# Performance work log

Measured on AMD Instinct MI355X. Metric: run time of the kernel, lower is better.

Reference implementation:

```python
import jax, jax.numpy as jnp
import numpy as np

B, N, D = 2048, 64, 256
DH = D // 2  # theta/phi projection dim
EPS = 1e-5

def layer_norm(x, g, b):
    m = jnp.mean(x, axis=-1, keepdims=True)
    v = jnp.var(x, axis=-1, keepdims=True)
    return (x - m) * jax.lax.rsqrt(v + EPS) * g + b

def graph_conv(x, adj, th_w, ph_w, fc_w, fc_b):
    # static adjacency: softmax over rows, shared across batch
    A_static = jax.nn.softmax(adj, axis=-1)  # [N, N]
    q = jnp.einsum('bnd,hd->bnh', x, th_w)   # [B, N, DH]
    k = jnp.einsum('bnd,hd->bnh', x, ph_w)   # [B, N, DH]
    scores = jnp.einsum('bni,bmi->bnm', q, k) / jnp.sqrt(jnp.asarray(DH, x.dtype))
    A_hat = A_static[None] + jax.nn.softmax(scores, axis=-1)  # [B, N, N]
    agg = jnp.einsum('bnm,bmd->bnd', A_hat, x)
    return jnp.einsum('bnd,od->bno', agg, fc_w) + fc_b

def setup_inputs() -> dict:
    key = jax.random.key(0)
    ks = jax.random.split(key, 12)
    eye = jnp.eye(N, dtype=jnp.float32)
    s = 1.0 / np.sqrt(D)
    return {
        'graph':  jax.random.normal(ks[0], (B, N, D), jnp.float32),
        'ln_in_g': jnp.ones((D,), jnp.float32), 'ln_in_b': jnp.zeros((D,), jnp.float32),
        'adj0':  eye + 0.01 * jax.random.normal(ks[1], (N, N), jnp.float32),
        'th0':   jax.random.uniform(ks[2], (DH, D), jnp.float32, -s, s),
        'ph0':   jax.random.uniform(ks[3], (DH, D), jnp.float32, -s, s),
        'fcw0':  jax.random.uniform(ks[4], (D, D), jnp.float32, -s, s),
        'fcb0':  jax.random.uniform(ks[5], (D,), jnp.float32, -s, s),
        'ln0_g': jnp.ones((D,), jnp.float32), 'ln0_b': jnp.zeros((D,), jnp.float32),
        'adj1':  eye + 0.01 * jax.random.normal(ks[6], (N, N), jnp.float32),
        'th1':   jax.random.uniform(ks[7], (DH, D), jnp.float32, -s, s),
        'ph1':   jax.random.uniform(ks[8], (DH, D), jnp.float32, -s, s),
        'fcw1':  jax.random.uniform(ks[9], (D, D), jnp.float32, -s, s),
        'fcb1':  jax.random.uniform(ks[10], (D,), jnp.float32, -s, s),
    }

def reference(graph, ln_in_g, ln_in_b, adj0, th0, ph0, fcw0, fcb0,
              ln0_g, ln0_b, adj1, th1, ph1, fcw1, fcb1):
    x = layer_norm(graph, ln_in_g, ln_in_b)
    x = graph_conv(x, adj0, th0, ph0, fcw0, fcb0)
    x = layer_norm(x, ln0_g, ln0_b)
    x = jnp.where(x >= 0, x, 0.1 * x)  # LeakyReLU(0.1); dropout is identity in eval
    x = graph_conv(x, adj1, th1, ph1, fcw1, fcb1)
    return x
```

## Files before the change

kernel.cpp:

```cpp
#include <hip/hip_runtime.h>

typedef __bf16 bf16x8 __attribute__((ext_vector_type(8)));
typedef __bf16 bf16x4 __attribute__((ext_vector_type(4)));
typedef float  f32x4  __attribute__((ext_vector_type(4)));

constexpr int WS_AS0 = 0;
constexpr int WS_AS1 = 4096;
constexpr int WS_TH0 = 8192;
constexpr int WS_PH0 = 40960;
constexpr int WS_FC0 = 73728;
constexpr int WS_TH1 = 139264;
constexpr int WS_PH1 = 172032;
constexpr int WS_FC1 = 204800;

static __device__ __forceinline__ f32x4 mfma16(bf16x8 a, bf16x8 b, f32x4 c) {
    return __builtin_amdgcn_mfma_f32_16x16x32_bf16(a, b, c, 0, 0, 0);
}

__global__ void prep_adj(const float* __restrict__ adj0,
                         const float* __restrict__ adj1,
                         __bf16* __restrict__ wsb) {
    const int t = threadIdx.x;
    const int l = t >> 6, r = t & 63;
    const float* a = (l ? adj1 : adj0) + r * 64;
    float mx = -3.0e38f;
    for (int c = 0; c < 64; ++c) mx = fmaxf(mx, a[c]);
    float s = 0.f;
    for (int c = 0; c < 64; ++c) s += __expf(a[c] - mx);
    const float inv = 1.f / s;
    __bf16* dst = wsb + (l ? WS_AS1 : WS_AS0) + r * 64;
    for (int c = 0; c < 64; ++c) dst[c] = (__bf16)(__expf(a[c] - mx) * inv);
}

__global__ void prep_w(const float* __restrict__ th0, const float* __restrict__ ph0,
                       const float* __restrict__ fc0, const float* __restrict__ th1,
                       const float* __restrict__ ph1, const float* __restrict__ fc1,
                       __bf16* __restrict__ wsb) {
    int i = blockIdx.x * 256 + threadIdx.x;
    if (i >= 262144) return;
    float v; int d;
    if      (i <  32768) { v = th0[i];          d = WS_TH0 + i;          }
    else if (i <  65536) { v = ph0[i -  32768]; d = WS_PH0 + i -  32768; }
    else if (i < 131072) { v = fc0[i -  65536]; d = WS_FC0 + i -  65536; }
    else if (i < 163840) { v = th1[i - 131072]; d = WS_TH1 + i - 131072; }
    else if (i < 196608) { v = ph1[i - 163840]; d = WS_PH1 + i - 163840; }
    else                 { v = fc1[i - 196608]; d = WS_FC1 + i - 196608; }
    wsb[d] = (__bf16)v;
}

__global__ __launch_bounds__(512, 4) void fused_gcn(
    const float* __restrict__ graph,
    const float* __restrict__ ln_in_g, const float* __restrict__ ln_in_b,
    const __bf16* __restrict__ wsb,
    const float* __restrict__ fcb0, const float* __restrict__ ln0_g,
    const float* __restrict__ ln0_b, const float* __restrict__ fcb1,
    float* __restrict__ outp)
{
    constexpr int XN_S = 264;
    constexpr int QK_S = 136;
    constexpr int ZT_S = 68;
    constexpr int AH_S = 72;

    __shared__ __align__(16) __bf16 sXn[64 * XN_S];
    __shared__ __align__(16) __bf16 sQKZ[2 * 64 * QK_S];
    __shared__ __align__(16) __bf16 sAh[64 * AH_S];
    __shared__ float sRed[128];

    const int tid = threadIdx.x;
    const int w = tid >> 6, lane = tid & 63;
    const int l15 = lane & 15, qd = lane >> 4;
    const int b = blockIdx.x;

    {
        const int r = tid >> 3, ci = (tid & 7) * 32;
        const float* gp = graph + (size_t)b * 16384 + r * 256 + ci;
        f32x4 v[8];
        float s = 0.f, s2 = 0.f;
        #pragma unroll
        for (int j = 0; j < 8; ++j) {
            v[j] = *(const f32x4*)(gp + j * 4);
            #pragma unroll
            for (int e = 0; e < 4; ++e) { s += v[j][e]; s2 += v[j][e] * v[j][e]; }
        }
        #pragma unroll
        for (int m = 1; m <= 4; m <<= 1) { s += __shfl_xor(s, m); s2 += __shfl_xor(s2, m); }
        const float mean = s * (1.f / 256.f);
        const float var  = s2 * (1.f / 256.f) - mean * mean;
        const float rstd = rsqrtf(var + 1e-5f);
        #pragma unroll
        for (int j = 0; j < 8; ++j) {
            f32x4 gg = *(const f32x4*)(ln_in_g + ci + j * 4);
            f32x4 bb = *(const f32x4*)(ln_in_b + ci + j * 4);
            bf16x4 pk;
            #pragma unroll
            for (int e = 0; e < 4; ++e)
                pk[e] = (__bf16)((v[j][e] - mean) * rstd * gg[e] + bb[e]);
            *(bf16x4*)&sXn[r * XN_S + ci + j * 4] = pk;
        }
    }
    __syncthreads();

    for (int layer = 0; layer < 2; ++layer) {
        const __bf16* As  = wsb + (layer ? WS_AS1 : WS_AS0);
        const __bf16* thb = wsb + (layer ? WS_TH1 : WS_TH0);
        const __bf16* phb = wsb + (layer ? WS_PH1 : WS_PH0);
        const __bf16* fcw = wsb + (layer ? WS_FC1 : WS_FC0);
        const float*  fcb = layer ? fcb1 : fcb0;

        {
            const int brow = w * 16 + l15;
            bf16x8 bth[8], bph[8];
            #pragma unroll
            for (int kk = 0; kk < 8; ++kk) {
                bth[kk] = *(const bf16x8*)(thb + brow * 256 + kk * 32 + qd * 8);
                bph[kk] = *(const bf16x8*)(phb + brow * 256 + kk * 32 + qd * 8);
            }
            #pragma unroll
            for (int m = 0; m < 4; ++m) {
                f32x4 aq = {0.f, 0.f, 0.f, 0.f}, ak = {0.f, 0.f, 0.f, 0.f};
                #pragma unroll
                for (int kk = 0; kk < 8; ++kk) {
                    bf16x8 a = *(const bf16x8*)&sXn[(m * 16 + l15) * XN_S + kk * 32 + qd * 8];
                    aq = mfma16(a, bth[kk], aq);
                    ak = mfma16(a, bph[kk], ak);
                }
                #pragma unroll
                for (int r = 0; r < 4; ++r) {
                    const int row = m * 16 + qd * 4 + r;
                    sQKZ[row * QK_S + w * 16 + l15]               = (__bf16)aq[r];
                    sQKZ[64 * QK_S + row * QK_S + w * 16 + l15]   = (__bf16)ak[r];
                }
            }
        }
        __syncthreads();

        if (w < 4) {
            const int mb = w * 16;
            bf16x8 aq[4];
            #pragma unroll
            for (int kk = 0; kk < 4; ++kk)
                aq[kk] = *(const bf16x8*)&sQKZ[(mb + l15) * QK_S + kk * 32 + qd * 8];
            f32x4 sc[4];
            #pragma unroll
            for (int nt = 0; nt < 4; ++nt) {
                f32x4 acc = {0.f, 0.f, 0.f, 0.f};
                #pragma unroll
                for (int kk = 0; kk < 4; ++kk) {
                    bf16x8 bk = *(const bf16x8*)&sQKZ[64 * QK_S + (nt * 16 + l15) * QK_S + kk * 32 + qd * 8];
                    acc = mfma16(aq[kk], bk, acc);
                }
                sc[nt] = acc;
            }
            const float scale = 0.088388347648318447f;
            #pragma unroll
            for (int r = 0; r < 4; ++r) {
                float v[4];
                #pragma unroll
                for (int nt = 0; nt < 4; ++nt) v[nt] = sc[nt][r] * scale;
                float mx = fmaxf(fmaxf(v[0], v[1]), fmaxf(v[2], v[3]));
                #pragma unroll
                for (int m = 1; m <= 8; m <<= 1) mx = fmaxf(mx, __shfl_xor(mx, m));
                float e[4], sum = 0.f;
                #pragma unroll
                for (int nt = 0; nt < 4; ++nt) { e[nt] = __expf(v[nt] - mx); sum += e[nt]; }
                #pragma unroll
                for (int m = 1; m <= 8; m <<= 1) sum += __shfl_xor(sum, m);
                const float inv = 1.f / sum;
                const int row = mb + qd * 4 + r;
                #pragma unroll
                for (int nt = 0; nt < 4; ++nt) {
                    const int col = nt * 16 + l15;
                    sAh[row * AH_S + col] = (__bf16)(e[nt] * inv + (float)As[row * 64 + col]);
                }
            }
        } else {
            const int i = tid - 256;
            if (i < 128) sRed[i] = 0.f;
        }
        __syncthreads();

        {
            bf16x8 bfc[2][8];
            #pragma unroll
            for (int j = 0; j < 2; ++j) {
                const int o = (w * 2 + j) * 16 + l15;
                #pragma unroll
                for (int kk = 0; kk < 8; ++kk)
                    bfc[j][kk] = *(const bf16x8*)(fcw + o * 256 + kk * 32 + qd * 8);
            }
            #pragma unroll
            for (int m = 0; m < 4; ++m) {
                f32x4 az0 = {0.f, 0.f, 0.f, 0.f}, az1 = {0.f, 0.f, 0.f, 0.f};
                #pragma unroll
                for (int kk = 0; kk < 8; ++kk) {
                    bf16x8 a = *(const bf16x8*)&sXn[(m * 16 + l15) * XN_S + kk * 32 + qd * 8];
                    az0 = mfma16(a, bfc[0][kk], az0);
                    az1 = mfma16(a, bfc[1][kk], az1);
                }
                #pragma unroll
                for (int j = 0; j < 2; ++j) {
                    const f32x4 az = j ? az1 : az0;
                    const int o = (w * 2 + j) * 16 + l15;
                    bf16x4 pk;
                    #pragma unroll
                    for (int r = 0; r < 4; ++r) pk[r] = (__bf16)az[r];
                    *(bf16x4*)&sQKZ[o * ZT_S + m * 16 + qd * 4] = pk;
                }
            }
        }
        __syncthreads();

        {
            const int mb = (w & 3) * 16, ng = w >> 2;
            bf16x8 aa[2];
            #pragma unroll
            for (int kk = 0; kk < 2; ++kk)
                aa[kk] = *(const bf16x8*)&sAh[(mb + l15) * AH_S + kk * 32 + qd * 8];
            f32x4 oacc[8];
            #pragma unroll
            for (int j = 0; j < 8; ++j) {
                const int o = ng * 128 + j * 16 + l15;
                f32x4 acc = {0.f, 0.f, 0.f, 0.f};
                #pragma unroll
                for (int kk = 0; kk < 2; ++kk) {
                    bf16x4 lo = *(const bf16x4*)&sQKZ[o * ZT_S + kk * 32 + qd * 8];
                    bf16x4 hi = *(const bf16x4*)&sQKZ[o * ZT_S + kk * 32 + qd * 8 + 4];
                    bf16x8 bb = __builtin_shufflevector(lo, hi, 0, 1, 2, 3, 4, 5, 6, 7);
                    acc = mfma16(aa[kk], bb, acc);
                }
                const float bias = fcb[o];
                #pragma unroll
                for (int r = 0; r < 4; ++r) acc[r] += bias;
                oacc[j] = acc;
            }

            if (layer == 0) {
                #pragma unroll
                for (int r = 0; r < 4; ++r) {
                    float s = 0.f, s2 = 0.f;
                    #pragma unroll
                    for (int j = 0; j < 8; ++j) { const float vv = oacc[j][r]; s += vv; s2 += vv * vv; }
                    #pragma unroll
                    for (int m = 1; m <= 8; m <<= 1) { s += __shfl_xor(s, m); s2 += __shfl_xor(s2, m); }
                    if (l15 == 0) {
                        const int row = mb + qd * 4 + r;
                        atomicAdd(&sRed[row], s);
                        atomicAdd(&sRed[64 + row], s2);
                    }
                }
                __syncthreads();
                float mean4[4], rstd4[4];
                #pragma unroll
                for (int r = 0; r < 4; ++r) {
                    const int row = mb + qd * 4 + r;
                    const float mean = sRed[row] * (1.f / 256.f);
                    const float var  = sRed[64 + row] * (1.f / 256.f) - mean * mean;
                    mean4[r] = mean;
                    rstd4[r] = rsqrtf(var + 1e-5f);
                }
                #pragma unroll
                for (int j = 0; j < 8; ++j) {
                    const int o = ng * 128 + j * 16 + l15;
                    const float g = ln0_g[o], bb = ln0_b[o];
                    #pragma unroll
                    for (int r = 0; r < 4; ++r) {
                        float y = (oacc[j][r] - mean4[r]) * rstd4[r] * g + bb;
                        y = (y >= 0.f) ? y : 0.1f * y;
                        sXn[(mb + qd * 4 + r) * XN_S + o] = (__bf16)y;
                    }
                }
                __syncthreads();
            } else {
                float* op = outp + (size_t)b * 16384;
                #pragma unroll
                for (int j = 0; j < 8; ++j) {
                    const int o = ng * 128 + j * 16 + l15;
                    #pragma unroll
                    for (int r = 0; r < 4; ++r)
                        op[(mb + qd * 4 + r) * 256 + o] = oacc[j][r];
                }
            }
        }
    }
}

extern "C" void kernel_launch(void* const* d_in, const int* in_sizes, int n_in,
                              void* d_out, int out_size, void* d_ws, size_t ws_size,
                              hipStream_t stream) {
    const float* graph   = (const float*)d_in[0];
    const float* ln_in_g = (const float*)d_in[1];
    const float* ln_in_b = (const float*)d_in[2];
    const float* adj0    = (const float*)d_in[3];
    const float* th0     = (const float*)d_in[4];
    const float* ph0     = (const float*)d_in[5];
    const float* fcw0    = (const float*)d_in[6];
    const float* fcb0    = (const float*)d_in[7];
    const float* ln0_g   = (const float*)d_in[8];
    const float* ln0_b   = (const float*)d_in[9];
    const float* adj1    = (const float*)d_in[10];
    const float* th1     = (const float*)d_in[11];
    const float* ph1     = (const float*)d_in[12];
    const float* fcw1    = (const float*)d_in[13];
    const float* fcb1    = (const float*)d_in[14];
    __bf16* wsb = (__bf16*)d_ws;

    prep_adj<<<1, 128, 0, stream>>>(adj0, adj1, wsb);
    prep_w<<<1024, 256, 0, stream>>>(th0, ph0, fcw0, th1, ph1, fcw1, wsb);
    fused_gcn<<<2048, 512, 0, stream>>>(graph, ln_in_g, ln_in_b, wsb,
                                        fcb0, ln0_g, ln0_b, fcb1, (float*)d_out);
}
```

Before: 422.8 us.

## Fold theta and phi weights into one scaled bilinear matrix per layer

```diff
diff --git a/kernel.cpp b/kernel.cpp
--- a/kernel.cpp
+++ b/kernel.cpp
@@ -6,11 +6,9 @@
 
 constexpr int WS_AS0 = 0;
 constexpr int WS_AS1 = 4096;
-constexpr int WS_TH0 = 8192;
-constexpr int WS_PH0 = 40960;
-constexpr int WS_FC0 = 73728;
-constexpr int WS_TH1 = 139264;
-constexpr int WS_PH1 = 172032;
+constexpr int WS_MT0 = 8192;
+constexpr int WS_MT1 = 73728;
+constexpr int WS_FC0 = 139264;
 constexpr int WS_FC1 = 204800;
 
 static __device__ __forceinline__ f32x4 mfma16(bf16x8 a, bf16x8 b, f32x4 c) {
@@ -32,20 +30,23 @@
     for (int c = 0; c < 64; ++c) dst[c] = (__bf16)(__expf(a[c] - mx) * inv);
 }
 
-__global__ void prep_w(const float* __restrict__ th0, const float* __restrict__ ph0,
-                       const float* __restrict__ fc0, const float* __restrict__ th1,
-                       const float* __restrict__ ph1, const float* __restrict__ fc1,
+__global__ void prep_M(const float* __restrict__ th0, const float* __restrict__ ph0,
+                       const float* __restrict__ th1, const float* __restrict__ ph1,
+                       __bf16* __restrict__ wsb) {
+    const int e = blockIdx.x & 255, layer = blockIdx.x >> 8, d = threadIdx.x;
+    const float* th = layer ? th1 : th0;
+    const float* ph = layer ? ph1 : ph0;
+    float s = 0.f;
+    for (int h = 0; h < 128; ++h) s += ph[h * 256 + e] * th[h * 256 + d];
+    wsb[(layer ? WS_MT1 : WS_MT0) + e * 256 + d] = (__bf16)(s * 0.088388347648318447f);
+}
+
+__global__ void prep_w(const float* __restrict__ fc0, const float* __restrict__ fc1,
                        __bf16* __restrict__ wsb) {
     int i = blockIdx.x * 256 + threadIdx.x;
-    if (i >= 262144) return;
-    float v; int d;
-    if      (i <  32768) { v = th0[i];          d = WS_TH0 + i;          }
-    else if (i <  65536) { v = ph0[i -  32768]; d = WS_PH0 + i -  32768; }
-    else if (i < 131072) { v = fc0[i -  65536]; d = WS_FC0 + i -  65536; }
-    else if (i < 163840) { v = th1[i - 131072]; d = WS_TH1 + i - 131072; }
-    else if (i < 196608) { v = ph1[i - 163840]; d = WS_PH1 + i - 163840; }
-    else                 { v = fc1[i - 196608]; d = WS_FC1 + i - 196608; }
-    wsb[d] = (__bf16)v;
+    if (i >= 131072) return;
+    if (i < 65536) wsb[WS_FC0 + i] = (__bf16)fc0[i];
+    else           wsb[WS_FC1 + i - 65536] = (__bf16)fc1[i - 65536];
 }
 
 __global__ __launch_bounds__(512, 4) void fused_gcn(
@@ -57,12 +58,11 @@
     float* __restrict__ outp)
 {
     constexpr int XN_S = 264;
-    constexpr int QK_S = 136;
-    constexpr int ZT_S = 68;
+    constexpr int ZT_S = 72;
     constexpr int AH_S = 72;
 
     __shared__ __align__(16) __bf16 sXn[64 * XN_S];
-    __shared__ __align__(16) __bf16 sQKZ[2 * 64 * QK_S];
+    __shared__ __align__(16) __bf16 sR1[256 * ZT_S];
     __shared__ __align__(16) __bf16 sAh[64 * AH_S];
     __shared__ float sRed[128];
 
@@ -72,6 +72,7 @@
     const int b = blockIdx.x;
 
     {
+        if (tid < 128) sRed[tid] = 0.f;
         const int r = tid >> 3, ci = (tid & 7) * 32;
         const float* gp = graph + (size_t)b * 16384 + r * 256 + ci;
         f32x4 v[8];
@@ -100,63 +101,67 @@
     }
     __syncthreads();
 
+    #pragma unroll
     for (int layer = 0; layer < 2; ++layer) {
         const __bf16* As  = wsb + (layer ? WS_AS1 : WS_AS0);
-        const __bf16* thb = wsb + (layer ? WS_TH1 : WS_TH0);
-        const __bf16* phb = wsb + (layer ? WS_PH1 : WS_PH0);
+        const __bf16* mtw = wsb + (layer ? WS_MT1 : WS_MT0);
         const __bf16* fcw = wsb + (layer ? WS_FC1 : WS_FC0);
         const float*  fcb = layer ? fcb1 : fcb0;
 
         {
-            const int brow = w * 16 + l15;
-            bf16x8 bth[8], bph[8];
-            #pragma unroll
-            for (int kk = 0; kk < 8; ++kk) {
-                bth[kk] = *(const bf16x8*)(thb + brow * 256 + kk * 32 + qd * 8);
-                bph[kk] = *(const bf16x8*)(phb + brow * 256 + kk * 32 + qd * 8);
-            }
-            #pragma unroll
-            for (int m = 0; m < 4; ++m) {
-                f32x4 aq = {0.f, 0.f, 0.f, 0.f}, ak = {0.f, 0.f, 0.f, 0.f};
+            bf16x8 amt[16];
+            #pragma unroll
+            for (int jm = 0; jm < 2; ++jm)
+                #pragma unroll
+                for (int kk = 0; kk < 8; ++kk)
+                    amt[jm * 8 + kk] = *(const bf16x8*)(mtw + ((w * 2 + jm) * 16 + l15) * 256 + kk * 32 + qd * 8);
+            f32x4 tacc[2][4];
+            #pragma unroll
+            for (int jm = 0; jm < 2; ++jm)
+                #pragma unroll
+                for (int nt = 0; nt < 4; ++nt) tacc[jm][nt] = (f32x4){0.f, 0.f, 0.f, 0.f};
+            #pragma unroll
+            for (int nt = 0; nt < 4; ++nt)
                 #pragma unroll
                 for (int kk = 0; kk < 8; ++kk) {
-                    bf16x8 a = *(const bf16x8*)&sXn[(m * 16 + l15) * XN_S + kk * 32 + qd * 8];
-                    aq = mfma16(a, bth[kk], aq);
-                    ak = mfma16(a, bph[kk], ak);
-                }
-                #pragma unroll
-                for (int r = 0; r < 4; ++r) {
-                    const int row = m * 16 + qd * 4 + r;
-                    sQKZ[row * QK_S + w * 16 + l15]               = (__bf16)aq[r];
-                    sQKZ[64 * QK_S + row * QK_S + w * 16 + l15]   = (__bf16)ak[r];
-                }
-            }
+                    bf16x8 bx = *(const bf16x8*)&sXn[(nt * 16 + l15) * XN_S + kk * 32 + qd * 8];
+                    tacc[0][nt] = mfma16(amt[kk], bx, tacc[0][nt]);
+                    tacc[1][nt] = mfma16(amt[8 + kk], bx, tacc[1][nt]);
+                }
+            #pragma unroll
+            for (int jm = 0; jm < 2; ++jm)
+                #pragma unroll
+                for (int nt = 0; nt < 4; ++nt) {
+                    bf16x4 pk;
+                    #pragma unroll
+                    for (int r = 0; r < 4; ++r) pk[r] = (__bf16)tacc[jm][nt][r];
+                    *(bf16x4*)&sR1[(nt * 16 + l15) * XN_S + (w * 2 + jm) * 16 + qd * 4] = pk;
+                }
         }
         __syncthreads();
 
+        bf16x4 zpk[16];
         if (w < 4) {
             const int mb = w * 16;
-            bf16x8 aq[4];
-            #pragma unroll
-            for (int kk = 0; kk < 4; ++kk)
-                aq[kk] = *(const bf16x8*)&sQKZ[(mb + l15) * QK_S + kk * 32 + qd * 8];
+            bf16x8 at[8];
+            #pragma unroll
+            for (int kk = 0; kk < 8; ++kk)
+                at[kk] = *(const bf16x8*)&sR1[(mb + l15) * XN_S + kk * 32 + qd * 8];
             f32x4 sc[4];
             #pragma unroll
-            for (int nt = 0; nt < 4; ++nt) {
-                f32x4 acc = {0.f, 0.f, 0.f, 0.f};
-                #pragma unroll
-                for (int kk = 0; kk < 4; ++kk) {
-                    bf16x8 bk = *(const bf16x8*)&sQKZ[64 * QK_S + (nt * 16 + l15) * QK_S + kk * 32 + qd * 8];
-                    acc = mfma16(aq[kk], bk, acc);
-                }
-                sc[nt] = acc;
-            }
-            const float scale = 0.088388347648318447f;
+            for (int nt = 0; nt < 4; ++nt) sc[nt] = (f32x4){0.f, 0.f, 0.f, 0.f};
+            #pragma unroll
+            for (int nt = 0; nt < 4; ++nt)
+                #pragma unroll
+                for (int kk = 0; kk < 8; ++kk) {
+                    bf16x8 bx = *(const bf16x8*)&sXn[(nt * 16 + l15) * XN_S + kk * 32 + qd * 8];
+                    sc[nt] = mfma16(at[kk], bx, sc[nt]);
+                }
             #pragma unroll
             for (int r = 0; r < 4; ++r) {
                 float v[4];
                 #pragma unroll
-                for (int nt = 0; nt < 4; ++nt) v[nt] = sc[nt][r] * scale;
+                for (int nt = 0; nt < 4; ++nt) v[nt] = sc[nt][r];
                 float mx = fmaxf(fmaxf(v[0], v[1]), fmaxf(v[2], v[3]));
                 #pragma unroll
                 for (int m = 1; m <= 8; m <<= 1) mx = fmaxf(mx, __shfl_xor(mx, m));
@@ -174,39 +179,34 @@
                 }
             }
         } else {
-            const int i = tid - 256;
-            if (i < 128) sRed[i] = 0.f;
+            const int mt = w - 4;
+            bf16x8 ax[8];
+            #pragma unroll
+            for (int kk = 0; kk < 8; ++kk)
+                ax[kk] = *(const bf16x8*)&sXn[(mt * 16 + l15) * XN_S + kk * 32 + qd * 8];
+            #pragma unroll
+            for (int ot = 0; ot < 16; ++ot) {
+                bf16x8 bfc[8];
+                #pragma unroll
+                for (int kk = 0; kk < 8; ++kk)
+                    bfc[kk] = *(const bf16x8*)(fcw + (ot * 16 + l15) * 256 + kk * 32 + qd * 8);
+                f32x4 a0 = {0.f, 0.f, 0.f, 0.f}, a1 = {0.f, 0.f, 0.f, 0.f};
+                #pragma unroll
+                for (int kk = 0; kk < 4; ++kk) {
+                    a0 = mfma16(ax[kk], bfc[kk], a0);
+                    a1 = mfma16(ax[4 + kk], bfc[4 + kk], a1);
+                }
+                #pragma unroll
+                for (int r = 0; r < 4; ++r) zpk[ot][r] = (__bf16)(a0[r] + a1[r]);
+            }
         }
         __syncthreads();
 
-        {
-            bf16x8 bfc[2][8];
-            #pragma unroll
-            for (int j = 0; j < 2; ++j) {
-                const int o = (w * 2 + j) * 16 + l15;
-                #pragma unroll
-                for (int kk = 0; kk < 8; ++kk)
-                    bfc[j][kk] = *(const bf16x8*)(fcw + o * 256 + kk * 32 + qd * 8);
-            }
-            #pragma unroll
-            for (int m = 0; m < 4; ++m) {
-                f32x4 az0 = {0.f, 0.f, 0.f, 0.f}, az1 = {0.f, 0.f, 0.f, 0.f};
-                #pragma unroll
-                for (int kk = 0; kk < 8; ++kk) {
-                    bf16x8 a = *(const bf16x8*)&sXn[(m * 16 + l15) * XN_S + kk * 32 + qd * 8];
-                    az0 = mfma16(a, bfc[0][kk], az0);
-                    az1 = mfma16(a, bfc[1][kk], az1);
-                }
-                #pragma unroll
-                for (int j = 0; j < 2; ++j) {
-                    const f32x4 az = j ? az1 : az0;
-                    const int o = (w * 2 + j) * 16 + l15;
-                    bf16x4 pk;
-                    #pragma unroll
-                    for (int r = 0; r < 4; ++r) pk[r] = (__bf16)az[r];
-                    *(bf16x4*)&sQKZ[o * ZT_S + m * 16 + qd * 4] = pk;
-                }
-            }
+        if (w >= 4) {
+            const int mt = w - 4;
+            #pragma unroll
+            for (int ot = 0; ot < 16; ++ot)
+                *(bf16x4*)&sR1[(ot * 16 + l15) * ZT_S + mt * 16 + qd * 4] = zpk[ot];
         }
         __syncthreads();
 
@@ -223,9 +223,7 @@
                 f32x4 acc = {0.f, 0.f, 0.f, 0.f};
                 #pragma unroll
                 for (int kk = 0; kk < 2; ++kk) {
-                    bf16x4 lo = *(const bf16x4*)&sQKZ[o * ZT_S + kk * 32 + qd * 8];
-                    bf16x4 hi = *(const bf16x4*)&sQKZ[o * ZT_S + kk * 32 + qd * 8 + 4];
-                    bf16x8 bb = __builtin_shufflevector(lo, hi, 0, 1, 2, 3, 4, 5, 6, 7);
+                    bf16x8 bb = *(const bf16x8*)&sR1[o * ZT_S + kk * 32 + qd * 8];
                     acc = mfma16(aa[kk], bb, acc);
                 }
                 const float bias = fcb[o];
@@ -305,7 +303,8 @@
     __bf16* wsb = (__bf16*)d_ws;
 
     prep_adj<<<1, 128, 0, stream>>>(adj0, adj1, wsb);
-    prep_w<<<1024, 256, 0, stream>>>(th0, ph0, fcw0, th1, ph1, fcw1, wsb);
+    prep_M<<<512, 256, 0, stream>>>(th0, ph0, th1, ph1, wsb);
+    prep_w<<<512, 256, 0, stream>>>(fcw0, fcw1, wsb);
     fused_gcn<<<2048, 512, 0, stream>>>(graph, ln_in_g, ln_in_b, wsb,
                                         fcb0, ln0_g, ln0_b, fcb1, (float*)d_out);
 }
```

After: 587.5 us. 1.39x slower.
